# Kernel optimization log

Measured on AMD Instinct MI355X. Metric: run time of the kernel, lower is better.

The kernel has to match this reference:

```python
import jax, jax.numpy as jnp
import numpy as np

CODEBOOK_SIZE = 8192
EMBED_DIM = 256


def setup_inputs() -> dict:
    key = jax.random.key(0)
    k1, k2 = jax.random.split(key)
    z = jax.random.normal(k1, (8, 4096, EMBED_DIM), dtype=jnp.float32)
    # matches torch init: uniform_(-1/codebook_size, 1/codebook_size)
    codebook = jax.random.uniform(
        k2, (CODEBOOK_SIZE, EMBED_DIM), dtype=jnp.float32,
        minval=-1.0 / CODEBOOK_SIZE, maxval=1.0 / CODEBOOK_SIZE)
    return {"z": z, "codebook": codebook}


def reference(z, codebook):
    # z: [B, S, D]; codebook: [K, D]
    z_flat = z.reshape(-1, z.shape[-1])                      # [N, D]
    # ||z||^2 - 2 z.E^T + ||E||^2  -> [N, K]
    distances = (
        jnp.sum(z_flat * z_flat, axis=1, keepdims=True)
        - 2.0 * jnp.einsum("nd,kd->nk", z_flat, codebook)
        + jnp.sum(codebook * codebook, axis=1)
    )
    encoding_indices = jnp.argmin(distances, axis=1)         # [N]
    z_q = codebook[encoding_indices].reshape(z.shape)        # [B, S, D]
    return z_q, encoding_indices
```

## Files before the change

### kernel.cpp

```cpp
#include <hip/hip_runtime.h>


#define NROWS 32768
#define DIM   256
#define KCB   8192
#define CANDCAP 128
#define MARGIN  4.5e-4f
#define WBUF    320

#define SB_CAND  0u
#define SB_CNT   8388608u
#define SB_ZSQ   8519680u
#define SB_CSQ   8650752u
#define SB_CSQ1  8683520u
#define SB_OVL   8716288u
#define SB_OVC   8847360u
#define SB_IMG   8847424u
#define SB_NEED  13041728u

using bf16x8 = __attribute__((ext_vector_type(8))) short;
using f32x4  = __attribute__((ext_vector_type(4))) float;
using u32x4  = __attribute__((ext_vector_type(4))) unsigned int;

__device__ __forceinline__ unsigned short bf16rne(float f) {
    unsigned u = __float_as_uint(f);
    unsigned r = u + 0x7FFFu + ((u >> 16) & 1u);
    return (unsigned short)(r >> 16);
}

__device__ __forceinline__ unsigned pack2_bf16(float a, float b) {
    return (unsigned)bf16rne(a) | ((unsigned)bf16rne(b) << 16);
}

__device__ float np_sumsq_256(const float* __restrict__ p) {
#pragma clang fp contract(off)
    float blk[2];
    #pragma unroll
    for (int b = 0; b < 2; ++b) {
        const float4* q4 = reinterpret_cast<const float4*>(p + b * 128);
        float4 a0 = q4[0], a1 = q4[1];
        float r[8];
        r[0] = __fmul_rn(a0.x, a0.x); r[1] = __fmul_rn(a0.y, a0.y);
        r[2] = __fmul_rn(a0.z, a0.z); r[3] = __fmul_rn(a0.w, a0.w);
        r[4] = __fmul_rn(a1.x, a1.x); r[5] = __fmul_rn(a1.y, a1.y);
        r[6] = __fmul_rn(a1.z, a1.z); r[7] = __fmul_rn(a1.w, a1.w);
        #pragma unroll
        for (int i = 2; i < 32; i += 2) {
            a0 = q4[i]; a1 = q4[i + 1];
            r[0] = __fadd_rn(r[0], __fmul_rn(a0.x, a0.x));
            r[1] = __fadd_rn(r[1], __fmul_rn(a0.y, a0.y));
            r[2] = __fadd_rn(r[2], __fmul_rn(a0.z, a0.z));
            r[3] = __fadd_rn(r[3], __fmul_rn(a0.w, a0.w));
            r[4] = __fadd_rn(r[4], __fmul_rn(a1.x, a1.x));
            r[5] = __fadd_rn(r[5], __fmul_rn(a1.y, a1.y));
            r[6] = __fadd_rn(r[6], __fmul_rn(a1.z, a1.z));
            r[7] = __fadd_rn(r[7], __fmul_rn(a1.w, a1.w));
        }
        blk[b] = __fadd_rn(
            __fadd_rn(__fadd_rn(r[0], r[1]), __fadd_rn(r[2], r[3])),
            __fadd_rn(__fadd_rn(r[4], r[5]), __fadd_rn(r[6], r[7])));
    }
    return __fadd_rn(blk[0], blk[1]);
}

__global__ void vq_prep_kernel(const float* __restrict__ z,
                               const float* __restrict__ cb,
                               char* __restrict__ img,
                               float* __restrict__ zsq, float* __restrict__ csq,
                               float* __restrict__ csq1,
                               unsigned* __restrict__ cnt, unsigned* __restrict__ ovc) {
    int t = blockIdx.x * 256 + threadIdx.x;
    if (t < NROWS) cnt[t] = 0;
    if (t == 0) *ovc = 0;
    if (t < 262144) {
        int s = t & 63, kk = (t >> 6) & 7, T = t >> 9;
        int code = s & 15, lhi = s >> 4;
        const float* src = cb + (size_t)(T * 16 + code) * DIM + kk * 32 + lhi * 8;
        float4 v0 = *reinterpret_cast<const float4*>(src);
        float4 v1 = *reinterpret_cast<const float4*>(src + 4);
        uint4 o;
        o.x = pack2_bf16(v0.x, v0.y); o.y = pack2_bf16(v0.z, v0.w);
        o.z = pack2_bf16(v1.x, v1.y); o.w = pack2_bf16(v1.z, v1.w);
        *reinterpret_cast<uint4*>(img + (size_t)T * 8192 + kk * 1024 + s * 16) = o;
    } else if (t < 262144 + KCB) {
        int k = t - 262144;
        float s = np_sumsq_256(cb + (size_t)k * DIM);
        csq[k] = s;
        csq1[k] = s + 1.0f;
    } else if (t < 262144 + KCB + NROWS) {
        int r = t - 262144 - KCB;
        zsq[r] = np_sumsq_256(z + (size_t)r * DIM);
    }
}

__global__ __launch_bounds__(512, 2) void vq_screen_kernel(
    const float* __restrict__ z, const char* __restrict__ img,
    const float* __restrict__ csq1,
    unsigned* __restrict__ cnt, unsigned short* __restrict__ cand) {
    __shared__ unsigned runmin[128];
    __shared__ unsigned wcnt[8];
    __shared__ unsigned wbuf[8][WBUF];
    const int tid = threadIdx.x, lane = tid & 63, wid = tid >> 6;
    const int wr = wid >> 2, wc = wid & 3;
    const int l15 = lane & 15, lhi = lane >> 4;
    const int row0 = blockIdx.x * 128;
    const int tbase = wc * 128;

    bf16x8 ah[4][8];
    #pragma unroll
    for (int m = 0; m < 4; ++m) {
        const float* zr = z + (size_t)(row0 + wr * 64 + m * 16 + l15) * DIM;
        #pragma unroll
        for (int kk = 0; kk < 8; ++kk) {
            float4 v0 = *reinterpret_cast<const float4*>(zr + kk * 32 + lhi * 8);
            float4 v1 = *reinterpret_cast<const float4*>(zr + kk * 32 + lhi * 8 + 4);
            uint4 o;
            o.x = pack2_bf16(v0.x, v0.y); o.y = pack2_bf16(v0.z, v0.w);
            o.z = pack2_bf16(v1.x, v1.y); o.w = pack2_bf16(v1.z, v1.w);
            ah[m][kk] = __builtin_bit_cast(bf16x8, o);
        }
    }

    if (tid < 128) runmin[tid] = 0x7F800000u;
    if (tid < 8) wcnt[tid] = 0;
    __syncthreads();

    f32x4 aA[4], aB[4];
    #pragma unroll
    for (int m = 0; m < 4; ++m) {
        aA[m] = (f32x4){0.f, 0.f, 0.f, 0.f};
        aB[m] = (f32x4){0.f, 0.f, 0.f, 0.f};
    }

    const char*  gp  = img + (size_t)tbase * 8192 + (size_t)lane * 16;
    const float* cpe = csq1 + tbase * 16 + l15;
    int codeb = tbase * 16 + l15;

    u32x4 bA[8], bB[8];

    auto PUSH = [&](int lr, int code) {
        unsigned pi = atomicAdd(&wcnt[wid], 1u);
        if (pi < WBUF) wbuf[wid][pi] = ((unsigned)lr << 13) | (unsigned)code;
        else {
            int grow = row0 + lr;
            unsigned gs = atomicAdd(&cnt[grow], 1u);
            if (gs < CANDCAP) cand[(size_t)grow * CANDCAP + gs] = (unsigned short)code;
        }
    };

#define LOADR(bh)                                                         \
    {                                                                     \
        _Pragma("unroll")                                                 \
        for (int kk = 0; kk < 8; ++kk)                                    \
            bh[kk] = *reinterpret_cast<const u32x4*>(gp + kk * 1024);     \
        gp += 8192;                                                       \
    }

#define MFMAS(bh, a)                                                      \
    {                                                                     \
        _Pragma("unroll")                                                 \
        for (int kk = 0; kk < 8; ++kk) {                                  \
            bf16x8 bv = __builtin_bit_cast(bf16x8, bh[kk]);               \
            _Pragma("unroll")                                             \
            for (int m = 0; m < 4; ++m)                                   \
                a[m] = __builtin_amdgcn_mfma_f32_16x16x32_bf16(           \
                    ah[m][kk], bv, a[m], 0, 0, 0);                        \
        }                                                                 \
    }

#define EPI(a)                                                            \
    {                                                                     \
        const float csv = *cpe; cpe += 16;                                \
        _Pragma("unroll")                                                 \
        for (int m = 0; m < 4; ++m) {                                     \
            const int lr0 = wr * 64 + m * 16 + lhi * 4;                   \
            uint4 rmb = *reinterpret_cast<const uint4*>(&runmin[lr0]);    \
            float s0 = fmaf(a[m][0], -2.0f, csv);                         \
            float s1 = fmaf(a[m][1], -2.0f, csv);                         \
            float s2 = fmaf(a[m][2], -2.0f, csv);                         \
            float s3 = fmaf(a[m][3], -2.0f, csv);                         \
            bool c0 = s0 < __uint_as_float(rmb.x) + MARGIN;               \
            bool c1 = s1 < __uint_as_float(rmb.y) + MARGIN;               \
            bool c2 = s2 < __uint_as_float(rmb.z) + MARGIN;               \
            bool c3 = s3 < __uint_as_float(rmb.w) + MARGIN;               \
            if (__any(c0 | c1 | c2 | c3)) {                               \
                if (c0) { if (s0 < __uint_as_float(rmb.x)) atomicMin(&runmin[lr0 + 0], __float_as_uint(s0)); PUSH(lr0 + 0, codeb); } \
                if (c1) { if (s1 < __uint_as_float(rmb.y)) atomicMin(&runmin[lr0 + 1], __float_as_uint(s1)); PUSH(lr0 + 1, codeb); } \
                if (c2) { if (s2 < __uint_as_float(rmb.z)) atomicMin(&runmin[lr0 + 2], __float_as_uint(s2)); PUSH(lr0 + 2, codeb); } \
                if (c3) { if (s3 < __uint_as_float(rmb.w)) atomicMin(&runmin[lr0 + 3], __float_as_uint(s3)); PUSH(lr0 + 3, codeb); } \
            }                                                             \
            a[m] = (f32x4){0.f, 0.f, 0.f, 0.f};                           \
        }                                                                 \
        codeb += 16;                                                      \
    }

    LOADR(bA);
    LOADR(bB);
    MFMAS(bA, aA);
    LOADR(bA);
    MFMAS(bB, aB);
    {
        const float csv = *cpe; cpe += 16;
        #pragma unroll
        for (int m = 0; m < 4; ++m) {
            const int lr0 = wr * 64 + m * 16 + lhi * 4;
            #pragma unroll
            for (int r = 0; r < 4; ++r) {
                float s2 = fmaf(aA[m][r], -2.0f, csv);
                float sm = s2;
                sm = fminf(sm, __shfl_xor(sm, 1));
                sm = fminf(sm, __shfl_xor(sm, 2));
                sm = fminf(sm, __shfl_xor(sm, 4));
                sm = fminf(sm, __shfl_xor(sm, 8));
                if (l15 == 0) atomicMin(&runmin[lr0 + r], __float_as_uint(sm));
                if (s2 < sm + MARGIN) PUSH(lr0 + r, codeb);
            }
            aA[m] = (f32x4){0.f, 0.f, 0.f, 0.f};
        }
        codeb += 16;
    }

    for (int i = 1; i <= 62; ++i) {
        LOADR(bB);  MFMAS(bA, aA);  EPI(aB);
        LOADR(bA);  MFMAS(bB, aB);  EPI(aA);
    }
    LOADR(bB);  MFMAS(bA, aA);  EPI(aB);
    MFMAS(bB, aB);  EPI(aA);
    EPI(aB);

    unsigned n = wcnt[wid]; if (n > WBUF) n = WBUF;
    for (unsigned e = lane; e < n; e += 64) {
        unsigned u = wbuf[wid][e];
        int row = row0 + (int)(u >> 13);
        int code = (int)(u & 8191u);
        unsigned slot = atomicAdd(&cnt[row], 1u);
        if (slot < CANDCAP) cand[(size_t)row * CANDCAP + slot] = (unsigned short)code;
    }
#undef LOADR
#undef MFMAS
#undef EPI
}

__global__ __launch_bounds__(256) void vq_exact_kernel(
    const float* __restrict__ z, const float* __restrict__ cb,
    const float* __restrict__ zsq, const float* __restrict__ csq,
    const unsigned* __restrict__ cnt, const unsigned short* __restrict__ cand,
    unsigned* __restrict__ ovl, unsigned* __restrict__ ovc,
    float* __restrict__ idxF, float4* __restrict__ outz, int fused) {
    __shared__ float zrow[4][DIM];
    const int wid = threadIdx.x >> 6, lane = threadIdx.x & 63;
    const int row = blockIdx.x * 4 + wid;

    float4 zv4 = *reinterpret_cast<const float4*>(&z[(size_t)row * DIM + lane * 4]);
    *reinterpret_cast<float4*>(&zrow[wid][lane * 4]) = zv4;
    __syncthreads();

    const unsigned c = cnt[row];
    if (c == 0 || c > CANDCAP) {
        if (lane == 0) { unsigned s = atomicAdd(ovc, 1u); ovl[s] = row; }
        return;
    }

    const float Zr = zsq[row];
    const float4* cb4 = reinterpret_cast<const float4*>(cb);
    float best = 3.4e38f;
    int   bi   = 0x7FFFFFFF;

    for (int j = lane; j < (int)c; j += 64) {
        int k = cand[(size_t)row * CANDCAP + j];
        float a = 0.0f;
        #pragma unroll 8
        for (int q = 0; q < 64; ++q) {
            float4 cv = cb4[(size_t)k * 64 + q];
            float4 zv = *reinterpret_cast<const float4*>(&zrow[wid][q * 4]);
            a = fmaf(zv.x, cv.x, a); a = fmaf(zv.y, cv.y, a);
            a = fmaf(zv.z, cv.z, a); a = fmaf(zv.w, cv.w, a);
        }
        float sv = __fadd_rn(__fsub_rn(Zr, __fmul_rn(2.0f, a)), csq[k]);
        if (sv < best || (sv == best && k < bi)) { best = sv; bi = k; }
    }
    #pragma unroll
    for (int mk = 32; mk >= 1; mk >>= 1) {
        float ov = __shfl_xor(best, mk);
        int   oi = __shfl_xor(bi, mk);
        if (ov < best || (ov == best && oi < bi)) { best = ov; bi = oi; }
    }
    if (lane == 0) idxF[row] = (float)bi;
    if (fused) outz[(size_t)row * 64 + lane] = cb4[(size_t)bi * 64 + lane];
}

__global__ __launch_bounds__(256) void vq_cleanup_kernel(
    const float* __restrict__ z, const float* __restrict__ cb,
    const float* __restrict__ zsq, const float* __restrict__ csq,
    const unsigned* __restrict__ ovl, const unsigned* __restrict__ ovc,
    float* __restrict__ idxF, float4* __restrict__ outz, int fused) {
    __shared__ float zrow[DIM];
    __shared__ float wv[4]; __shared__ int wi[4];
    __shared__ int sbi;
    const int lane = threadIdx.x & 63, wid = threadIdx.x >> 6;
    const unsigned count = *ovc;
    for (unsigned w = blockIdx.x; w < count; w += gridDim.x) {
        const int row = ovl[w];
        __syncthreads();
        *reinterpret_cast<float4*>(&zrow[threadIdx.x * 4 & (DIM - 1)]) =
            *reinterpret_cast<const float4*>(&z[(size_t)row * DIM + (threadIdx.x * 4 & (DIM - 1))]);
        __syncthreads();
        const float Zr = zsq[row];
        const float4* cb4 = reinterpret_cast<const float4*>(cb);
        float best = 3.4e38f; int bi = 0x7FFFFFFF;
        for (int k = threadIdx.x; k < KCB; k += 256) {
            float a = 0.0f;
            #pragma unroll 8
            for (int q = 0; q < 64; ++q) {
                float4 cv = cb4[(size_t)k * 64 + q];
                float4 zv = *reinterpret_cast<const float4*>(&zrow[q * 4]);
                a = fmaf(zv.x, cv.x, a); a = fmaf(zv.y, cv.y, a);
                a = fmaf(zv.z, cv.z, a); a = fmaf(zv.w, cv.w, a);
            }
            float sv = __fadd_rn(__fsub_rn(Zr, __fmul_rn(2.0f, a)), csq[k]);
            if (sv < best || (sv == best && k < bi)) { best = sv; bi = k; }
        }
        #pragma unroll
        for (int mk = 32; mk >= 1; mk >>= 1) {
            float ov = __shfl_xor(best, mk);
            int   oi = __shfl_xor(bi, mk);
            if (ov < best || (ov == best && oi < bi)) { best = ov; bi = oi; }
        }
        if (lane == 0) { wv[wid] = best; wi[wid] = bi; }
        __syncthreads();
        if (threadIdx.x == 0) {
            #pragma unroll
            for (int u = 1; u < 4; ++u)
                if (wv[u] < best || (wv[u] == best && wi[u] < bi)) { best = wv[u]; bi = wi[u]; }
            idxF[row] = (float)bi;
            sbi = bi;
        }
        __syncthreads();
        if (fused && threadIdx.x < 64)
            outz[(size_t)row * 64 + threadIdx.x] = cb4[(size_t)sbi * 64 + threadIdx.x];
    }
}

__global__ void vq_gather_kernel(const float* __restrict__ cb,
                                 const float* __restrict__ idxF,
                                 float4* __restrict__ out4) {
    int g = blockIdx.x * blockDim.x + threadIdx.x;
    const float4* cb4 = reinterpret_cast<const float4*>(cb);
    for (int i = g; i < NROWS * 64; i += gridDim.x * blockDim.x) {
        int row = i >> 6, q = i & 63;
        int idx = (int)idxF[row];
        out4[i] = cb4[(size_t)idx * 64 + q];
    }
}

extern "C" void kernel_launch(void* const* d_in, const int* in_sizes, int n_in,
                              void* d_out, int out_size, void* d_ws, size_t ws_size,
                              hipStream_t stream) {
    const float* z  = (const float*)d_in[0];
    const float* cb = (const float*)d_in[1];
    float* out = (float*)d_out;

    const int fused = (ws_size >= (size_t)SB_NEED) ? 1 : 0;
    char* SB = fused ? (char*)d_ws : (char*)d_out;

    unsigned short* candp = (unsigned short*)(SB + SB_CAND);
    unsigned*       cntp  = (unsigned*)(SB + SB_CNT);
    float*          zsq   = (float*)(SB + SB_ZSQ);
    float*          csq   = (float*)(SB + SB_CSQ);
    float*          csq1  = (float*)(SB + SB_CSQ1);
    unsigned*       ovl   = (unsigned*)(SB + SB_OVL);
    unsigned*       ovc   = (unsigned*)(SB + SB_OVC);
    char*           img   = SB + SB_IMG;
    float*          idxF  = out + 8388608;

    vq_prep_kernel<<<(262144 + KCB + NROWS + 255) / 256, 256, 0, stream>>>(
        z, cb, img, zsq, csq, csq1, cntp, ovc);
    vq_screen_kernel<<<NROWS / 128, 512, 0, stream>>>(z, img, csq1, cntp, candp);
    vq_exact_kernel<<<NROWS / 4, 256, 0, stream>>>(
        z, cb, zsq, csq, cntp, candp, ovl, ovc, idxF, (float4*)out, fused);
    vq_cleanup_kernel<<<64, 256, 0, stream>>>(
        z, cb, zsq, csq, ovl, ovc, idxF, (float4*)out, fused);
    if (!fused)
        vq_gather_kernel<<<2048, 256, 0, stream>>>(cb, idxF, (float4*)out);
}
```

Baseline: 292.1 us.

## Triple-buffer codebook tile loads and use a single accumulator set

Replaces the two-accumulator ping-pong schedule with a single accumulator and three register buffers for codebook tiles, so global loads are issued two tiles ahead of the MFMA consumption. The epilogue now runs directly after each tile's MFMAs instead of overlapping with the other accumulator's MFMAs. This aims to hide global load latency better, at the cost of more VGPRs for the extra B buffer and a serialized MFMA to epilogue dependency.

Result: slower. 300.7 us (+2.9%).

```diff
diff --git a/kernel.cpp b/kernel.cpp
--- a/kernel.cpp
+++ b/kernel.cpp
@@ -125,18 +125,15 @@
     if (tid < 8) wcnt[tid] = 0;
     __syncthreads();
 
-    f32x4 aA[4], aB[4];
+    f32x4 acc[4];
     #pragma unroll
-    for (int m = 0; m < 4; ++m) {
-        aA[m] = (f32x4){0.f, 0.f, 0.f, 0.f};
-        aB[m] = (f32x4){0.f, 0.f, 0.f, 0.f};
-    }
+    for (int m = 0; m < 4; ++m) acc[m] = (f32x4){0.f, 0.f, 0.f, 0.f};
 
     const char*  gp  = img + (size_t)tbase * 8192 + (size_t)lane * 16;
     const float* cpe = csq1 + tbase * 16 + l15;
     int codeb = tbase * 16 + l15;
 
-    u32x4 bA[8], bB[8];
+    u32x4 bA[8], bB[8], bC[8];
 
     auto PUSH = [&](int lr, int code) {
         unsigned pi = atomicAdd(&wcnt[wid], 1u);
@@ -156,29 +153,29 @@
         gp += 8192;                                                       \
     }
 
-#define MFMAS(bh, a)                                                      \
+#define MFMAS(bh)                                                         \
     {                                                                     \
         _Pragma("unroll")                                                 \
         for (int kk = 0; kk < 8; ++kk) {                                  \
             bf16x8 bv = __builtin_bit_cast(bf16x8, bh[kk]);               \
             _Pragma("unroll")                                             \
             for (int m = 0; m < 4; ++m)                                   \
-                a[m] = __builtin_amdgcn_mfma_f32_16x16x32_bf16(           \
-                    ah[m][kk], bv, a[m], 0, 0, 0);                        \
+                acc[m] = __builtin_amdgcn_mfma_f32_16x16x32_bf16(         \
+                    ah[m][kk], bv, acc[m], 0, 0, 0);                      \
         }                                                                 \
     }
 
-#define EPI(a)                                                            \
+#define EPI()                                                             \
     {                                                                     \
         const float csv = *cpe; cpe += 16;                                \
         _Pragma("unroll")                                                 \
         for (int m = 0; m < 4; ++m) {                                     \
             const int lr0 = wr * 64 + m * 16 + lhi * 4;                   \
             uint4 rmb = *reinterpret_cast<const uint4*>(&runmin[lr0]);    \
-            float s0 = fmaf(a[m][0], -2.0f, csv);                         \
-            float s1 = fmaf(a[m][1], -2.0f, csv);                         \
-            float s2 = fmaf(a[m][2], -2.0f, csv);                         \
-            float s3 = fmaf(a[m][3], -2.0f, csv);                         \
+            float s0 = fmaf(acc[m][0], -2.0f, csv);                       \
+            float s1 = fmaf(acc[m][1], -2.0f, csv);                       \
+            float s2 = fmaf(acc[m][2], -2.0f, csv);                       \
+            float s3 = fmaf(acc[m][3], -2.0f, csv);                       \
             bool c0 = s0 < __uint_as_float(rmb.x) + MARGIN;               \
             bool c1 = s1 < __uint_as_float(rmb.y) + MARGIN;               \
             bool c2 = s2 < __uint_as_float(rmb.z) + MARGIN;               \
@@ -189,16 +186,15 @@
                 if (c2) { if (s2 < __uint_as_float(rmb.z)) atomicMin(&runmin[lr0 + 2], __float_as_uint(s2)); PUSH(lr0 + 2, codeb); } \
                 if (c3) { if (s3 < __uint_as_float(rmb.w)) atomicMin(&runmin[lr0 + 3], __float_as_uint(s3)); PUSH(lr0 + 3, codeb); } \
             }                                                             \
-            a[m] = (f32x4){0.f, 0.f, 0.f, 0.f};                           \
+            acc[m] = (f32x4){0.f, 0.f, 0.f, 0.f};                         \
         }                                                                 \
         codeb += 16;                                                      \
     }
 
     LOADR(bA);
     LOADR(bB);
-    MFMAS(bA, aA);
-    LOADR(bA);
-    MFMAS(bB, aB);
+    LOADR(bC);
+    MFMAS(bA);
     {
         const float csv = *cpe; cpe += 16;
         #pragma unroll
@@ -206,7 +202,7 @@
             const int lr0 = wr * 64 + m * 16 + lhi * 4;
             #pragma unroll
             for (int r = 0; r < 4; ++r) {
-                float s2 = fmaf(aA[m][r], -2.0f, csv);
+                float s2 = fmaf(acc[m][r], -2.0f, csv);
                 float sm = s2;
                 sm = fminf(sm, __shfl_xor(sm, 1));
                 sm = fminf(sm, __shfl_xor(sm, 2));
@@ -215,18 +211,20 @@
                 if (l15 == 0) atomicMin(&runmin[lr0 + r], __float_as_uint(sm));
                 if (s2 < sm + MARGIN) PUSH(lr0 + r, codeb);
             }
-            aA[m] = (f32x4){0.f, 0.f, 0.f, 0.f};
+            acc[m] = (f32x4){0.f, 0.f, 0.f, 0.f};
         }
         codeb += 16;
     }
 
-    for (int i = 1; i <= 62; ++i) {
-        LOADR(bB);  MFMAS(bA, aA);  EPI(aB);
-        LOADR(bA);  MFMAS(bB, aB);  EPI(aA);
-    }
-    LOADR(bB);  MFMAS(bA, aA);  EPI(aB);
-    MFMAS(bB, aB);  EPI(aA);
-    EPI(aB);
+    for (int g = 0; g < 41; ++g) {
+        LOADR(bA);  MFMAS(bB);  EPI();
+        LOADR(bB);  MFMAS(bC);  EPI();
+        LOADR(bC);  MFMAS(bA);  EPI();
+    }
+    LOADR(bA);  MFMAS(bB);  EPI();
+    LOADR(bB);  MFMAS(bC);  EPI();
+    MFMAS(bA);  EPI();
+    MFMAS(bB);  EPI();
 
     unsigned n = wcnt[wid]; if (n > WBUF) n = WBUF;
     for (unsigned e = lane; e < n; e += 64) {
```
